# Kernel tuning notes

Measured on AMD Instinct MI355X. Metric: run time of the kernel, lower is better.

The kernel has to match this reference:

```python
import jax, jax.numpy as jnp
import numpy as np

ROPE_THETA = 10000.0


def _rope(x, pos, theta):
    # x: [B, H, S, d_k], pos: [S] int. Interleaved RoPE (pairs (2i, 2i+1)).
    d_k = x.shape[-1]
    inv_freq = theta ** (-2.0 * jnp.arange(d_k // 2, dtype=jnp.float32) / d_k)  # [d_k/2]
    ang = pos.astype(jnp.float32)[:, None] * inv_freq  # [S, d_k/2]
    cos, sin = jnp.cos(ang), jnp.sin(ang)
    xe, xo = x[..., 0::2], x[..., 1::2]
    re = xe * cos - xo * sin
    ro = xe * sin + xo * cos
    return jnp.stack([re, ro], axis=-1).reshape(x.shape)


def setup_inputs() -> dict:
    key = jax.random.key(0)
    ks = jax.random.split(key, 5)
    B, S, D = 2, 2048, 1024
    return {
        "in_features": jax.random.normal(ks[0], (B, S, D), jnp.float32),
        "q_proj_weight": jax.random.normal(ks[1], (D, D), jnp.float32) * (D ** -0.5),
        "k_proj_weight": jax.random.normal(ks[2], (D, D), jnp.float32) * (D ** -0.5),
        "v_proj_weight": jax.random.normal(ks[3], (D, D), jnp.float32) * (D ** -0.5),
        "o_proj_weight": jax.random.normal(ks[4], (D, D), jnp.float32) * (D ** -0.5),
        "token_positions": jnp.arange(S, dtype=jnp.int64),
        "d_model": 1024,
        "num_heads": 16,
    }


def reference(in_features, q_proj_weight, k_proj_weight, v_proj_weight,
              o_proj_weight, token_positions, d_model, num_heads):
    B, S, _ = in_features.shape
    d_k = d_model // num_heads

    def split_heads(x):  # [B, S, D] -> [B, H, S, d_k]
        return x.reshape(B, S, num_heads, d_k).transpose(0, 2, 1, 3)

    q = split_heads(in_features @ q_proj_weight.T)
    k = split_heads(in_features @ k_proj_weight.T)
    v = split_heads(in_features @ v_proj_weight.T)

    q = _rope(q, token_positions, ROPE_THETA)
    k = _rope(k, token_positions, ROPE_THETA)

    scores = jnp.einsum("bhqd,bhkd->bhqk", q, k) / jnp.sqrt(jnp.float32(d_k))
    causal = token_positions[:, None] >= token_positions[None, :]  # [S, S]
    scores = jnp.where(causal, scores, -jnp.inf)
    probs = jax.nn.softmax(scores, axis=-1)
    ctx = jnp.einsum("bhqk,bhkd->bhqd", probs, v)  # [B, H, S, d_k]
    ctx = ctx.transpose(0, 2, 1, 3).reshape(B, S, d_model)
    return ctx @ o_proj_weight.T
```

## Files before the change

### kernel.cpp

```cpp
#include <hip/hip_runtime.h>
#include <math.h>

typedef _Float16 f16;
typedef _Float16 f16x8 __attribute__((ext_vector_type(8)));
typedef float    f32x4 __attribute__((ext_vector_type(4)));

#define SEQ  2048
#define DM   1024
#define NH   16
#define DK   64
#define MTOT 4096

#define LOG2E 1.4426950408889634f

__global__ __launch_bounds__(256)
void cvt_all(const float* __restrict__ X,  const float* __restrict__ W0,
             const float* __restrict__ W1, const float* __restrict__ W2,
             const float* __restrict__ W3, f16* __restrict__ dst)
{
    const int i = (blockIdx.x * 256 + threadIdx.x) * 4;
    const float* src;
    if (i < (4 << 20)) {
        src = X + i;
    } else {
        const int j   = i - (4 << 20);
        const int sel = j >> 20;
        const float* W = (sel == 0) ? W0 : (sel == 1) ? W1 : (sel == 2) ? W2 : W3;
        src = W + (j & ((1 << 20) - 1));
    }
    float4 v = *(const float4*)src;
    f16 o[4] = {(f16)v.x, (f16)v.y, (f16)v.z, (f16)v.w};
    *(uint2*)&dst[i] = *(const uint2*)o;
}

__global__ __launch_bounds__(256)
void rope_table(float2* __restrict__ rt)
{
    const int i = blockIdx.x * 256 + threadIdx.x;
    const int s = i >> 5, p = i & 31;
    const float ang = (float)s * exp2f(-0.4152410118609203f * (float)p);
    float sn, cs;
    sincosf(ang, &sn, &cs);
    rt[i] = make_float2(cs, sn);
}

__global__ __launch_bounds__(512)
void gemm_qkv(const f16* __restrict__ A, const f16* __restrict__ W,
              f16* __restrict__ C, const float2* __restrict__ rt)
{
    __shared__ f16 As[128][72];
    __shared__ f16 Bs[128][72];

    const int tid  = threadIdx.x;
    const int wid  = tid >> 6, lane = tid & 63;
    const int l15  = lane & 15, l4 = lane >> 4;
    const int wm   = wid >> 2, wn = wid & 3;
    const int bm   = blockIdx.x * 128;
    const int sel  = blockIdx.y >> 3;
    const int bn   = (blockIdx.y & 7) * 128;
    const f16* B   = W + ((size_t)sel << 20);
    f16* Cb        = C + ((size_t)sel << 22);

    f32x4 acc[4][2];
    #pragma unroll
    for (int mi = 0; mi < 4; ++mi)
        #pragma unroll
        for (int ni = 0; ni < 2; ++ni)
            acc[mi][ni] = (f32x4){0.f, 0.f, 0.f, 0.f};

    for (int k0 = 0; k0 < DM; k0 += 64) {
        #pragma unroll
        for (int t = 0; t < 2; ++t) {
            const int li  = tid + t * 512;
            const int row = li >> 3, c8 = (li & 7) * 8;
            *(f16x8*)&As[row][c8] = *(const f16x8*)&A[(size_t)(bm + row) * DM + k0 + c8];
            *(f16x8*)&Bs[row][c8] = *(const f16x8*)&B[(size_t)(bn + row) * DM + k0 + c8];
        }
        __syncthreads();
        #pragma unroll
        for (int kc = 0; kc < 2; ++kc) {
            f16x8 af[4], bf[2];
            #pragma unroll
            for (int mi = 0; mi < 4; ++mi)
                af[mi] = *(const f16x8*)&As[wm*64 + mi*16 + l15][kc*32 + l4*8];
            #pragma unroll
            for (int ni = 0; ni < 2; ++ni)
                bf[ni] = *(const f16x8*)&Bs[wn*32 + ni*16 + l15][kc*32 + l4*8];
            #pragma unroll
            for (int mi = 0; mi < 4; ++mi)
                #pragma unroll
                for (int ni = 0; ni < 2; ++ni)
                    acc[mi][ni] = __builtin_amdgcn_mfma_f32_16x16x32_f16(
                        af[mi], bf[ni], acc[mi][ni], 0, 0, 0);
        }
        __syncthreads();
    }

    #pragma unroll
    for (int mi = 0; mi < 4; ++mi)
        #pragma unroll
        for (int ni = 0; ni < 2; ++ni)
            #pragma unroll
            for (int r = 0; r < 4; ++r) {
                const int row = bm + wm*64 + mi*16 + l4*4 + r;
                const int col = bn + wn*32 + ni*16 + l15;
                float v = acc[mi][ni][r];
                if (sel < 2) {
                    const float p   = __shfl_xor(v, 1);
                    const float2 cs = rt[((row & (SEQ-1)) << 5) | ((col & 63) >> 1)];
                    v = (col & 1) ? fmaf(v, cs.x,  p * cs.y)
                                  : fmaf(v, cs.x, -p * cs.y);
                }
                Cb[(size_t)row * DM + col] = (f16)v;
            }
}

__global__ __launch_bounds__(512)
void gemm_h(const f16* __restrict__ A, const f16* __restrict__ B,
            float* __restrict__ C)
{
    __shared__ f16 As[128][72];
    __shared__ f16 Bs[128][72];

    const int tid  = threadIdx.x;
    const int wid  = tid >> 6, lane = tid & 63;
    const int l15  = lane & 15, l4 = lane >> 4;
    const int wm   = wid >> 2, wn = wid & 3;
    const int bm   = blockIdx.x * 128, bn = blockIdx.y * 128;

    f32x4 acc[4][2];
    #pragma unroll
    for (int mi = 0; mi < 4; ++mi)
        #pragma unroll
        for (int ni = 0; ni < 2; ++ni)
            acc[mi][ni] = (f32x4){0.f, 0.f, 0.f, 0.f};

    for (int k0 = 0; k0 < DM; k0 += 64) {
        #pragma unroll
        for (int t = 0; t < 2; ++t) {
            const int li  = tid + t * 512;
            const int row = li >> 3, c8 = (li & 7) * 8;
            *(f16x8*)&As[row][c8] = *(const f16x8*)&A[(size_t)(bm + row) * DM + k0 + c8];
            *(f16x8*)&Bs[row][c8] = *(const f16x8*)&B[(size_t)(bn + row) * DM + k0 + c8];
        }
        __syncthreads();
        #pragma unroll
        for (int kc = 0; kc < 2; ++kc) {
            f16x8 af[4], bf[2];
            #pragma unroll
            for (int mi = 0; mi < 4; ++mi)
                af[mi] = *(const f16x8*)&As[wm*64 + mi*16 + l15][kc*32 + l4*8];
            #pragma unroll
            for (int ni = 0; ni < 2; ++ni)
                bf[ni] = *(const f16x8*)&Bs[wn*32 + ni*16 + l15][kc*32 + l4*8];
            #pragma unroll
            for (int mi = 0; mi < 4; ++mi)
                #pragma unroll
                for (int ni = 0; ni < 2; ++ni)
                    acc[mi][ni] = __builtin_amdgcn_mfma_f32_16x16x32_f16(
                        af[mi], bf[ni], acc[mi][ni], 0, 0, 0);
        }
        __syncthreads();
    }

    #pragma unroll
    for (int mi = 0; mi < 4; ++mi)
        #pragma unroll
        for (int ni = 0; ni < 2; ++ni)
            #pragma unroll
            for (int r = 0; r < 4; ++r) {
                const int row = bm + wm*64 + mi*16 + l4*4 + r;
                const int col = bn + wn*32 + ni*16 + l15;
                C[(size_t)row * DM + col] = acc[mi][ni][r];
            }
}

__global__ __launch_bounds__(256)
void flash_mfma(const f16* __restrict__ Q, const f16* __restrict__ K,
                const f16* __restrict__ V, f16* __restrict__ O)
{
    __shared__ f16 Ks [64][72];
    __shared__ f16 Vts[64][72];
    __shared__ f16 Ps [64][72];

    const int bh  = blockIdx.y, b = bh >> 4, h = bh & 15;
    const int tid = threadIdx.x, wid = tid >> 6, lane = tid & 63;
    const int l15 = lane & 15, l4 = lane >> 4;
    const size_t base = ((size_t)b * SEQ) * DM + h * DK;

    const int srow0 = tid >> 3,        sc8 = (tid & 7) * 8;
    const int srow1 = (tid + 256) >> 3;
    const int spc0  = srow0 ^ ((tid & 7) << 3);
    const int spc1  = srow1 ^ ((tid & 7) << 3);

    f16x8 kreg[2], vreg[2];

    #pragma unroll 1
    for (int qsel = 0; qsel < 2; ++qsel) {
        const int qt = qsel ? (31 - (int)blockIdx.x) : (int)blockIdx.x;

        f16x8 qf[2];
        {
            const size_t qrow = (size_t)(qt*64 + wid*16 + l15);
            #pragma unroll
            for (int kc = 0; kc < 2; ++kc) {
                qf[kc] = *(const f16x8*)&Q[base + qrow * DM + kc*32 + l4*8];
                #pragma unroll
                for (int j = 0; j < 8; ++j)
                    qf[kc][j] = (f16)((float)qf[kc][j] * (0.125f * LOG2E));
            }
        }

        float m_r[4], l_r[4];
        f32x4 acc_o[4];
        #pragma unroll
        for (int r = 0; r < 4; ++r) { m_r[r] = -INFINITY; l_r[r] = 0.f; }
        #pragma unroll
        for (int dg = 0; dg < 4; ++dg) acc_o[dg] = (f32x4){0.f, 0.f, 0.f, 0.f};

        {
            const size_t g0 = base + (size_t)(srow0) * DM + sc8;
            const size_t g1 = base + (size_t)(srow1) * DM + sc8;
            kreg[0] = *(const f16x8*)&K[g0]; vreg[0] = *(const f16x8*)&V[g0];
            kreg[1] = *(const f16x8*)&K[g1]; vreg[1] = *(const f16x8*)&V[g1];
        }
        __syncthreads();
        *(f16x8*)&Ks[srow0][sc8] = kreg[0];
        *(f16x8*)&Ks[srow1][sc8] = kreg[1];
        #pragma unroll
        for (int j = 0; j < 8; ++j) { Vts[sc8+j][spc0] = vreg[0][j];
                                      Vts[sc8+j][spc1] = vreg[1][j]; }
        __syncthreads();

        for (int kt = 0; kt <= qt; ++kt) {
            if (kt < qt) {
                const size_t g0 = base + (size_t)((kt+1)*64 + srow0) * DM + sc8;
                const size_t g1 = base + (size_t)((kt+1)*64 + srow1) * DM + sc8;
                kreg[0] = *(const f16x8*)&K[g0]; vreg[0] = *(const f16x8*)&V[g0];
                kreg[1] = *(const f16x8*)&K[g1]; vreg[1] = *(const f16x8*)&V[g1];
            }

            f32x4 sc[4];
            #pragma unroll
            for (int cg = 0; cg < 4; ++cg) sc[cg] = (f32x4){0.f, 0.f, 0.f, 0.f};
            #pragma unroll
            for (int cg = 0; cg < 4; ++cg)
                #pragma unroll
                for (int kc = 0; kc < 2; ++kc) {
                    f16x8 bf = *(const f16x8*)&Ks[cg*16 + l15][kc*32 + l4*8];
                    sc[cg] = __builtin_amdgcn_mfma_f32_16x16x32_f16(qf[kc], bf, sc[cg], 0, 0, 0);
                }

            if (kt == qt) {
                #pragma unroll
                for (int cg = 0; cg < 4; ++cg)
                    #pragma unroll
                    for (int r = 0; r < 4; ++r)
                        if (cg*16 + l15 > wid*16 + l4*4 + r) sc[cg][r] = -INFINITY;
            }

            #pragma unroll
            for (int r = 0; r < 4; ++r) {
                float mx = fmaxf(fmaxf(sc[0][r], sc[1][r]), fmaxf(sc[2][r], sc[3][r]));
                mx = fmaxf(mx, __shfl_xor(mx, 1));
                mx = fmaxf(mx, __shfl_xor(mx, 2));
                mx = fmaxf(mx, __shfl_xor(mx, 4));
                mx = fmaxf(mx, __shfl_xor(mx, 8));
                const float mn   = fmaxf(m_r[r], mx);
                const float corr = exp2f(m_r[r] - mn);
                float ps = 0.f;
                #pragma unroll
                for (int cg = 0; cg < 4; ++cg) {
                    const float pv = exp2f(sc[cg][r] - mn);
                    sc[cg][r] = pv;
                    ps += pv;
                }
                ps += __shfl_xor(ps, 1);
                ps += __shfl_xor(ps, 2);
                ps += __shfl_xor(ps, 4);
                ps += __shfl_xor(ps, 8);
                l_r[r] = l_r[r] * corr + ps;
                m_r[r] = mn;
                #pragma unroll
                for (int dg = 0; dg < 4; ++dg) acc_o[dg][r] *= corr;
            }

            #pragma unroll
            for (int cg = 0; cg < 4; ++cg)
                #pragma unroll
                for (int r = 0; r < 4; ++r)
                    Ps[wid*16 + l4*4 + r][cg*16 + l15] = (f16)sc[cg][r];

            #pragma unroll
            for (int kc = 0; kc < 2; ++kc) {
                f16x8 pa = *(const f16x8*)&Ps[wid*16 + l15][kc*32 + l4*8];
                #pragma unroll
                for (int dg = 0; dg < 4; ++dg) {
                    const int d   = dg*16 + l15;
                    const int pcr = (kc*32 + l4*8) ^ (((d >> 3) & 7) << 3);
                    f16x8 vb = *(const f16x8*)&Vts[d][pcr];
                    acc_o[dg] = __builtin_amdgcn_mfma_f32_16x16x32_f16(pa, vb, acc_o[dg], 0, 0, 0);
                }
            }

            __syncthreads();
            if (kt < qt) {
                *(f16x8*)&Ks[srow0][sc8] = kreg[0];
                *(f16x8*)&Ks[srow1][sc8] = kreg[1];
                #pragma unroll
                for (int j = 0; j < 8; ++j) { Vts[sc8+j][spc0] = vreg[0][j];
                                              Vts[sc8+j][spc1] = vreg[1][j]; }
            }
            __syncthreads();
        }

        #pragma unroll
        for (int dg = 0; dg < 4; ++dg)
            #pragma unroll
            for (int r = 0; r < 4; ++r) {
                const size_t row = (size_t)(qt*64 + wid*16 + l4*4 + r);
                O[base + row * DM + dg*16 + l15] = (f16)(acc_o[dg][r] / l_r[r]);
            }
    }
}

extern "C" void kernel_launch(void* const* d_in, const int* in_sizes, int n_in,
                              void* d_out, int out_size, void* d_ws, size_t ws_size,
                              hipStream_t stream)
{
    const float* X  = (const float*)d_in[0];
    const float* Wq = (const float*)d_in[1];
    const float* Wk = (const float*)d_in[2];
    const float* Wv = (const float*)d_in[3];
    const float* Wo = (const float*)d_in[4];

    f16* ws = (f16*)d_ws;
    const size_t M1 = 1u << 20;
    f16* Xh  = ws;
    f16* Wqh = ws + 4*M1;
    f16* Woh = ws + 7*M1;
    f16* Qh  = ws + 8*M1;
    f16* Kh  = ws + 12*M1;
    f16* Vh  = ws + 16*M1;
    f16* Ch  = ws + 20*M1;
    float2* rt = (float2*)(ws + 24*M1);

    cvt_all<<<8192, 256, 0, stream>>>(X, Wq, Wk, Wv, Wo, Xh);
    rope_table<<<256, 256, 0, stream>>>(rt);

    gemm_qkv<<<dim3(MTOT/128, 24), 512, 0, stream>>>(Xh, Wqh, Qh, rt);

    flash_mfma<<<dim3(16, NH*2), 256, 0, stream>>>(Qh, Kh, Vh, Ch);

    gemm_h<<<dim3(MTOT/128, DM/128), 512, 0, stream>>>(Ch, Woh, (float*)d_out);
}
```

Baseline: 229.5 us.

## Split flash attention KV tiles across two wave groups with merge

Each flash attention block now runs 512 threads as two groups of four waves. The groups take alternating KV tiles for the same 64 query rows, then merge their partial softmax states (max, sum, accumulator) through shared memory before writing output. The launch becomes a 1D grid remapped so that heads sharing an XCD stay together, which aims at L2 locality. This doubles per-block parallelism and shortens the serial KV loop per block. The cost is more shared memory, an extra merge step with barriers, and idle waves in a group when the tile count is odd.

```diff
diff --git a/kernel.cpp b/kernel.cpp
--- a/kernel.cpp
+++ b/kernel.cpp
@@ -175,33 +175,44 @@
             }
 }
 
-__global__ __launch_bounds__(256)
+__global__ __launch_bounds__(512)
 void flash_mfma(const f16* __restrict__ Q, const f16* __restrict__ K,
                 const f16* __restrict__ V, f16* __restrict__ O)
 {
-    __shared__ f16 Ks [64][72];
-    __shared__ f16 Vts[64][72];
-    __shared__ f16 Ps [64][72];
-
-    const int bh  = blockIdx.y, b = bh >> 4, h = bh & 15;
+    __shared__ f16 smem[6][64][72];
+
+    const int bid = blockIdx.x;
+    const int xcd = bid & 7, slot = bid >> 3;
+    const int bh  = xcd * 4 + (slot >> 4);
+    const int bx  = slot & 15;
+    const int b   = bh >> 4, h = bh & 15;
+
     const int tid = threadIdx.x, wid = tid >> 6, lane = tid & 63;
+    const int grp = wid >> 2, w4 = wid & 3;
     const int l15 = lane & 15, l4 = lane >> 4;
     const size_t base = ((size_t)b * SEQ) * DM + h * DK;
 
-    const int srow0 = tid >> 3,        sc8 = (tid & 7) * 8;
-    const int srow1 = (tid + 256) >> 3;
-    const int spc0  = srow0 ^ ((tid & 7) << 3);
-    const int spc1  = srow1 ^ ((tid & 7) << 3);
+    f16 (*Ks)[72]  = smem[grp];
+    f16 (*Vts)[72] = smem[2 + grp];
+    f16 (*Ps)[72]  = smem[4 + grp];
+
+    const int t256  = tid & 255;
+    const int srow0 = t256 >> 3,        sc8 = (t256 & 7) * 8;
+    const int srow1 = (t256 + 256) >> 3;
+    const int spc0  = srow0 ^ ((t256 & 7) << 3);
+    const int spc1  = srow1 ^ ((t256 & 7) << 3);
 
     f16x8 kreg[2], vreg[2];
 
     #pragma unroll 1
     for (int qsel = 0; qsel < 2; ++qsel) {
-        const int qt = qsel ? (31 - (int)blockIdx.x) : (int)blockIdx.x;
+        const int qt     = qsel ? (31 - bx) : bx;
+        const int ntiles = qt + 1;
+        const int tmax   = (ntiles + 1) >> 1;
 
         f16x8 qf[2];
         {
-            const size_t qrow = (size_t)(qt*64 + wid*16 + l15);
+            const size_t qrow = (size_t)(qt*64 + w4*16 + l15);
             #pragma unroll
             for (int kc = 0; kc < 2; ++kc) {
                 qf[kc] = *(const f16x8*)&Q[base + qrow * DM + kc*32 + l4*8];
@@ -218,93 +229,101 @@
         #pragma unroll
         for (int dg = 0; dg < 4; ++dg) acc_o[dg] = (f32x4){0.f, 0.f, 0.f, 0.f};
 
-        {
-            const size_t g0 = base + (size_t)(srow0) * DM + sc8;
-            const size_t g1 = base + (size_t)(srow1) * DM + sc8;
+        if (grp < ntiles) {
+            const size_t g0 = base + (size_t)(grp*64 + srow0) * DM + sc8;
+            const size_t g1 = base + (size_t)(grp*64 + srow1) * DM + sc8;
             kreg[0] = *(const f16x8*)&K[g0]; vreg[0] = *(const f16x8*)&V[g0];
             kreg[1] = *(const f16x8*)&K[g1]; vreg[1] = *(const f16x8*)&V[g1];
         }
         __syncthreads();
-        *(f16x8*)&Ks[srow0][sc8] = kreg[0];
-        *(f16x8*)&Ks[srow1][sc8] = kreg[1];
-        #pragma unroll
-        for (int j = 0; j < 8; ++j) { Vts[sc8+j][spc0] = vreg[0][j];
-                                      Vts[sc8+j][spc1] = vreg[1][j]; }
-        __syncthreads();
-
-        for (int kt = 0; kt <= qt; ++kt) {
-            if (kt < qt) {
-                const size_t g0 = base + (size_t)((kt+1)*64 + srow0) * DM + sc8;
-                const size_t g1 = base + (size_t)((kt+1)*64 + srow1) * DM + sc8;
+        if (grp < ntiles) {
+            *(f16x8*)&Ks[srow0][sc8] = kreg[0];
+            *(f16x8*)&Ks[srow1][sc8] = kreg[1];
+            #pragma unroll
+            for (int j = 0; j < 8; ++j) { Vts[sc8+j][spc0] = vreg[0][j];
+                                          Vts[sc8+j][spc1] = vreg[1][j]; }
+        }
+        __syncthreads();
+
+        for (int t = 0; t < tmax; ++t) {
+            const int  myt = 2*t + grp;
+            const bool act = myt < ntiles;
+            const int  nxt = myt + 2;
+
+            if (nxt < ntiles) {
+                const size_t g0 = base + (size_t)(nxt*64 + srow0) * DM + sc8;
+                const size_t g1 = base + (size_t)(nxt*64 + srow1) * DM + sc8;
                 kreg[0] = *(const f16x8*)&K[g0]; vreg[0] = *(const f16x8*)&V[g0];
                 kreg[1] = *(const f16x8*)&K[g1]; vreg[1] = *(const f16x8*)&V[g1];
             }
 
-            f32x4 sc[4];
-            #pragma unroll
-            for (int cg = 0; cg < 4; ++cg) sc[cg] = (f32x4){0.f, 0.f, 0.f, 0.f};
-            #pragma unroll
-            for (int cg = 0; cg < 4; ++cg)
+            if (act) {
+                f32x4 sc[4];
+                #pragma unroll
+                for (int cg = 0; cg < 4; ++cg) sc[cg] = (f32x4){0.f, 0.f, 0.f, 0.f};
+                #pragma unroll
+                for (int cg = 0; cg < 4; ++cg)
+                    #pragma unroll
+                    for (int kc = 0; kc < 2; ++kc) {
+                        f16x8 bf = *(const f16x8*)&Ks[cg*16 + l15][kc*32 + l4*8];
+                        sc[cg] = __builtin_amdgcn_mfma_f32_16x16x32_f16(qf[kc], bf, sc[cg], 0, 0, 0);
+                    }
+
+                if (myt == qt) {
+                    #pragma unroll
+                    for (int cg = 0; cg < 4; ++cg)
+                        #pragma unroll
+                        for (int r = 0; r < 4; ++r)
+                            if (cg*16 + l15 > w4*16 + l4*4 + r) sc[cg][r] = -INFINITY;
+                }
+
+                #pragma unroll
+                for (int r = 0; r < 4; ++r) {
+                    float mx = fmaxf(fmaxf(sc[0][r], sc[1][r]), fmaxf(sc[2][r], sc[3][r]));
+                    mx = fmaxf(mx, __shfl_xor(mx, 1));
+                    mx = fmaxf(mx, __shfl_xor(mx, 2));
+                    mx = fmaxf(mx, __shfl_xor(mx, 4));
+                    mx = fmaxf(mx, __shfl_xor(mx, 8));
+                    const float mn   = fmaxf(m_r[r], mx);
+                    const float corr = exp2f(m_r[r] - mn);
+                    float ps = 0.f;
+                    #pragma unroll
+                    for (int cg = 0; cg < 4; ++cg) {
+                        const float pv = exp2f(sc[cg][r] - mn);
+                        sc[cg][r] = pv;
+                        ps += pv;
+                    }
+                    ps += __shfl_xor(ps, 1);
+                    ps += __shfl_xor(ps, 2);
+                    ps += __shfl_xor(ps, 4);
+                    ps += __shfl_xor(ps, 8);
+                    l_r[r] = l_r[r] * corr + ps;
+                    m_r[r] = mn;
+                    #pragma unroll
+                    for (int dg = 0; dg < 4; ++dg) acc_o[dg][r] *= corr;
+                }
+
+                #pragma unroll
+                for (int cg = 0; cg < 4; ++cg)
+                    #pragma unroll
+                    for (int r = 0; r < 4; ++r)
+                        Ps[w4*16 + l4*4 + r][cg*16 + l15] = (f16)sc[cg][r];
+
                 #pragma unroll
                 for (int kc = 0; kc < 2; ++kc) {
-                    f16x8 bf = *(const f16x8*)&Ks[cg*16 + l15][kc*32 + l4*8];
-                    sc[cg] = __builtin_amdgcn_mfma_f32_16x16x32_f16(qf[kc], bf, sc[cg], 0, 0, 0);
+                    f16x8 pa = *(const f16x8*)&Ps[w4*16 + l15][kc*32 + l4*8];
+                    #pragma unroll
+                    for (int dg = 0; dg < 4; ++dg) {
+                        const int d   = dg*16 + l15;
+                        const int pcr = (kc*32 + l4*8) ^ (((d >> 3) & 7) << 3);
+                        f16x8 vb = *(const f16x8*)&Vts[d][pcr];
+                        acc_o[dg] = __builtin_amdgcn_mfma_f32_16x16x32_f16(pa, vb, acc_o[dg], 0, 0, 0);
+                    }
                 }
-
-            if (kt == qt) {
-                #pragma unroll
-                for (int cg = 0; cg < 4; ++cg)
-                    #pragma unroll
-                    for (int r = 0; r < 4; ++r)
-                        if (cg*16 + l15 > wid*16 + l4*4 + r) sc[cg][r] = -INFINITY;
-            }
-
-            #pragma unroll
-            for (int r = 0; r < 4; ++r) {
-                float mx = fmaxf(fmaxf(sc[0][r], sc[1][r]), fmaxf(sc[2][r], sc[3][r]));
-                mx = fmaxf(mx, __shfl_xor(mx, 1));
-                mx = fmaxf(mx, __shfl_xor(mx, 2));
-                mx = fmaxf(mx, __shfl_xor(mx, 4));
-                mx = fmaxf(mx, __shfl_xor(mx, 8));
-                const float mn   = fmaxf(m_r[r], mx);
-                const float corr = exp2f(m_r[r] - mn);
-                float ps = 0.f;
-                #pragma unroll
-                for (int cg = 0; cg < 4; ++cg) {
-                    const float pv = exp2f(sc[cg][r] - mn);
-                    sc[cg][r] = pv;
-                    ps += pv;
-                }
-                ps += __shfl_xor(ps, 1);
-                ps += __shfl_xor(ps, 2);
-                ps += __shfl_xor(ps, 4);
-                ps += __shfl_xor(ps, 8);
-                l_r[r] = l_r[r] * corr + ps;
-                m_r[r] = mn;
-                #pragma unroll
-                for (int dg = 0; dg < 4; ++dg) acc_o[dg][r] *= corr;
-            }
-
-            #pragma unroll
-            for (int cg = 0; cg < 4; ++cg)
-                #pragma unroll
-                for (int r = 0; r < 4; ++r)
-                    Ps[wid*16 + l4*4 + r][cg*16 + l15] = (f16)sc[cg][r];
-
-            #pragma unroll
-            for (int kc = 0; kc < 2; ++kc) {
-                f16x8 pa = *(const f16x8*)&Ps[wid*16 + l15][kc*32 + l4*8];
-                #pragma unroll
-                for (int dg = 0; dg < 4; ++dg) {
-                    const int d   = dg*16 + l15;
-                    const int pcr = (kc*32 + l4*8) ^ (((d >> 3) & 7) << 3);
-                    f16x8 vb = *(const f16x8*)&Vts[d][pcr];
-                    acc_o[dg] = __builtin_amdgcn_mfma_f32_16x16x32_f16(pa, vb, acc_o[dg], 0, 0, 0);
-                }
             }
 
             __syncthreads();
-            if (kt < qt) {
+            if (nxt < ntiles) {
                 *(f16x8*)&Ks[srow0][sc8] = kreg[0];
                 *(f16x8*)&Ks[srow1][sc8] = kreg[1];
                 #pragma unroll
@@ -314,13 +333,39 @@
             __syncthreads();
         }
 
-        #pragma unroll
-        for (int dg = 0; dg < 4; ++dg)
+        float* accx = (float*)&smem[0][0][0];
+        float* mlx  = (float*)&smem[4][0][0];
+
+        if (grp == 1) {
             #pragma unroll
             for (int r = 0; r < 4; ++r) {
-                const size_t row = (size_t)(qt*64 + wid*16 + l4*4 + r);
-                O[base + row * DM + dg*16 + l15] = (f16)(acc_o[dg][r] / l_r[r]);
-            }
+                const int ql = w4*16 + l4*4 + r;
+                mlx[ql]      = m_r[r];
+                mlx[64 + ql] = l_r[r];
+                #pragma unroll
+                for (int dg = 0; dg < 4; ++dg)
+                    accx[ql*64 + dg*16 + l15] = acc_o[dg][r];
+            }
+        }
+        __syncthreads();
+        if (grp == 0) {
+            #pragma unroll
+            for (int r = 0; r < 4; ++r) {
+                const int ql = w4*16 + l4*4 + r;
+                const float m1 = mlx[ql], l1 = mlx[64 + ql];
+                const float m  = fmaxf(m_r[r], m1);
+                const float c0 = exp2f(m_r[r] - m);
+                const float c1 = exp2f(m1 - m);
+                const float inv = 1.f / (l_r[r]*c0 + l1*c1);
+                const size_t row = (size_t)(qt*64 + ql);
+                #pragma unroll
+                for (int dg = 0; dg < 4; ++dg) {
+                    const float a1 = accx[ql*64 + dg*16 + l15];
+                    O[base + row * DM + dg*16 + l15] =
+                        (f16)((acc_o[dg][r]*c0 + a1*c1) * inv);
+                }
+            }
+        }
     }
 }
 
@@ -350,7 +395,7 @@
 
     gemm_qkv<<<dim3(MTOT/128, 24), 512, 0, stream>>>(Xh, Wqh, Qh, rt);
 
-    flash_mfma<<<dim3(16, NH*2), 256, 0, stream>>>(Qh, Kh, Vh, Ch);
+    flash_mfma<<<512, 512, 0, stream>>>(Qh, Kh, Vh, Ch);
 
     gemm_h<<<dim3(MTOT/128, DM/128), 512, 0, stream>>>(Ch, Woh, (float*)d_out);
 }
```

After: 233.4 us. About the same (+1.7%).
